# Optimization experiments

Hardware: AMD Instinct MI355X
Metric: run time of the kernel (lower is better)

Reference implementation:

```python
import jax, jax.numpy as jnp
import numpy as np

N = 50000        # nodes
E = 800000       # edges
FEAT = 64        # cfg.feature_dim
HID = 128        # cfg.hidden_dim
G = 8            # num graphs
EPS = 1e-5       # LayerNorm eps
MIN_DEPTH, MAX_DEPTH = 0.1, 3.0


def _ln(x, g, b):
    m = jnp.mean(x, axis=-1, keepdims=True)
    v = jnp.mean((x - m) ** 2, axis=-1, keepdims=True)
    return (x - m) * jax.lax.rsqrt(v + EPS) * g + b


def setup_inputs() -> dict:
    key = jax.random.key(0)
    ks = jax.random.split(key, 32)
    f32 = jnp.float32
    inp = {}
    inp['x'] = jax.random.normal(ks[0], (N, FEAT), dtype=f32)
    inp['edge_index'] = jax.random.randint(ks[1], (2, E), 0, N)
    inp['batch'] = jnp.sort(jax.random.randint(ks[2], (N,), 0, G))
    # input_projection: Linear(FEAT,HID) + LayerNorm
    inp['in_w'] = jax.random.normal(ks[3], (FEAT, HID), dtype=f32) * (1.0 / np.sqrt(FEAT))
    inp['in_b'] = jnp.zeros((HID,), f32)
    inp['in_ln_g'] = jnp.ones((HID,), f32)
    inp['in_ln_b'] = jnp.zeros((HID,), f32)
    # epigenetics
    inp['methylation'] = jnp.zeros((HID,), f32)
    inp['histones'] = jnp.zeros((4,), f32)
    inp['log_depth'] = jnp.zeros((), f32)
    # NeuralODEFunc: 3 stacked GCNConv(HID,HID) + LayerNorms, gate MLP, residual scalar
    inp['gcn_w'] = jax.random.normal(ks[4], (3, HID, HID), dtype=f32) * (1.0 / np.sqrt(HID))
    inp['gcn_b'] = jnp.zeros((3, HID), f32)
    inp['ln_g'] = jnp.ones((3, HID), f32)
    inp['ln_b'] = jnp.zeros((3, HID), f32)
    inp['gate_w'] = jax.random.normal(ks[5], (2 * HID, HID), dtype=f32) * (1.0 / np.sqrt(2 * HID))
    inp['gate_b'] = jnp.zeros((HID,), f32)
    inp['residual_weight'] = jnp.asarray(0.1, f32)
    # output_projection: Linear(HID,HID) + LayerNorm
    inp['out_w'] = jax.random.normal(ks[6], (HID, HID), dtype=f32) * (1.0 / np.sqrt(HID))
    inp['out_b'] = jnp.zeros((HID,), f32)
    inp['out_ln_g'] = jnp.ones((HID,), f32)
    inp['out_ln_b'] = jnp.zeros((HID,), f32)
    return inp


def reference(x, edge_index, batch, in_w, in_b, in_ln_g, in_ln_b, methylation,
              histones, log_depth, gcn_w, gcn_b, ln_g, ln_b, gate_w, gate_b,
              residual_weight, out_w, out_b, out_ln_g, out_ln_b):
    n = x.shape[0]
    src, dst = edge_index[0], edge_index[1]

    # input_projection (Dropout is identity in eval)
    h = jax.nn.relu(_ln(x @ in_w + in_b, in_ln_g, in_ln_b))

    # epigenetic regulation (chromatin_accessibility goes through .item() -> constant)
    meth_sil = jnp.mean(jax.nn.sigmoid(methylation))
    hm = jax.nn.sigmoid(histones)
    act = (hm[0] + hm[2]) * 0.5
    rep = (hm[1] + hm[3]) * 0.5
    chrom = jax.lax.stop_gradient(jnp.clip(act - rep + 0.5, 0.0, 1.0))
    h = h * (chrom * (1.0 - meth_sil))

    # symmetric GCN normalization, no self loops (computed once, no grad path)
    deg = jax.ops.segment_sum(jnp.ones((E,), h.dtype), dst, num_segments=n)
    dinv = jnp.where(deg > 0, jax.lax.rsqrt(jnp.maximum(deg, 1.0)), 0.0)
    enorm = (dinv[src] * dinv[dst])[:, None]  # [E,1]

    def gcn(hh, i):
        xw = hh @ gcn_w[i]                                   # [N,H]
        agg = jax.ops.segment_sum(xw[src] * enorm, dst, num_segments=n)
        return agg + gcn_b[i]

    def ode_f(hh):
        h_orig = hh
        cur = hh
        for i in range(3):  # fixed layer count
            h_new = _ln(gcn(cur, i), ln_g[i], ln_b[i])
            if i > 0:
                gate = jax.nn.sigmoid(
                    jnp.concatenate([cur, h_new], axis=-1) @ gate_w + gate_b)
                cur = gate * h_new + (1.0 - gate) * cur
            else:
                cur = h_new
        cur = jnp.tanh(cur)
        return cur + residual_weight * h_orig

    # depth via .item() in torch -> non-differentiable constant
    depth = jax.lax.stop_gradient(
        jnp.clip(jnp.exp(log_depth), MIN_DEPTH, MAX_DEPTH))
    # single fixed RK4 step over t = linspace(0, depth, 2)
    dt = depth
    k1 = ode_f(h)
    k2 = ode_f(h + 0.5 * dt * k1)
    k3 = ode_f(h + 0.5 * dt * k2)
    k4 = ode_f(h + dt * k3)
    h_final = h + (dt / 6.0) * (k1 + 2.0 * k2 + 2.0 * k3 + k4)

    # output_projection + global_mean_pool over batch
    h_out = _ln(h_final @ out_w + out_b, out_ln_g, out_ln_b)
    cnt = jax.ops.segment_sum(jnp.ones((n,), h.dtype), batch, num_segments=G)
    pooled = jax.ops.segment_sum(h_out, batch, num_segments=G)
    return pooled / jnp.maximum(cnt, 1.0)[:, None]
```

## Files before the change

kernel.cpp:

```cpp
#include <hip/hip_runtime.h>
#include <math.h>

#define NN 50000
#define EE 800000
#define HH 128
#define FF 64
#define GG 8
#define PB 500
#define SB 1600

using short8 = __attribute__((ext_vector_type(8))) short;
using f32x4  = __attribute__((ext_vector_type(4))) float;
using f32x2  = __attribute__((ext_vector_type(2))) float;

__device__ __forceinline__ float sigm(float x){ return 1.0f/(1.0f+expf(-x)); }
__device__ __forceinline__ unsigned short f2bf(float f){
    union { float f; unsigned u; } v; v.f = f;
    unsigned r = v.u + 0x7fff + ((v.u >> 16) & 1);
    return (unsigned short)(r >> 16);
}
__device__ __forceinline__ float bf2f(unsigned short h){
    union { unsigned u; float f; } v; v.u = ((unsigned)h) << 16;
    return v.f;
}

#if __has_builtin(__builtin_amdgcn_cvt_pk_fp8_f32) && __has_builtin(__builtin_amdgcn_cvt_pk_f32_fp8)
#define FP8_HW 1
#else
#define FP8_HW 0
#endif

__device__ __forceinline__ unsigned fp8enc1_sw(float f){
    union { float fl; unsigned u; } x; x.fl = f;
    unsigned s = (x.u >> 31) << 7;
    float a = fabsf(f);
    if (!(a > 0.f)) return s;
    if (a >= 448.f) return s | 0x7E;
    if (a < 0.015625f) {
        int q = (int)(a * 512.f + 0.5f);
        if (q > 7) return s | (1u << 3);
        return s | (unsigned)q;
    }
    unsigned u = x.u + (1u << 19);
    int e32 = (int)((u >> 23) & 255) - 127;
    if (e32 < -6) { int q=(int)(a*512.f+0.5f); if(q>7)q=7; return s|(unsigned)q; }
    if (e32 > 8) return s | 0x7E;
    unsigned m = (u >> 20) & 7;
    return s | ((unsigned)(e32 + 7) << 3) | m;
}
__device__ __forceinline__ float fp8dec1_sw(unsigned v){
    unsigned s = v >> 7, e = (v >> 3) & 15, m = v & 7;
    float f;
    if (e == 0) f = (float)m * 0.001953125f;
    else { union { unsigned u; float fl; } x; x.u = ((e + 120u) << 23) | (m << 20); f = x.fl; }
    return s ? -f : f;
}
__device__ __forceinline__ unsigned char e2fp8(float a){
#if FP8_HW
    return (unsigned char)(__builtin_amdgcn_cvt_pk_fp8_f32(a, a, 0, false) & 0xFF);
#else
    return (unsigned char)fp8enc1_sw(a);
#endif
}
__device__ __forceinline__ unsigned pk4fp8(float a, float b, float c, float d){
#if FP8_HW
    unsigned p0 = (unsigned)__builtin_amdgcn_cvt_pk_fp8_f32(a, b, 0, false);
    unsigned p1 = (unsigned)__builtin_amdgcn_cvt_pk_fp8_f32(c, d, 0, false);
    return (p0 & 0xFFFFu) | ((p1 & 0xFFFFu) << 16);
#else
    return fp8enc1_sw(a) | (fp8enc1_sw(b) << 8) | (fp8enc1_sw(c) << 16) | (fp8enc1_sw(d) << 24);
#endif
}
__device__ __forceinline__ float2 d2fp8(unsigned short u){
#if FP8_HW
    f32x2 r = __builtin_amdgcn_cvt_pk_f32_fp8((int)(unsigned)u, false);
    return make_float2(r[0], r[1]);
#else
    return make_float2(fp8dec1_sw(u & 0xFF), fp8dec1_sw((u >> 8) & 0xFF));
#endif
}

__global__ void k_setup(const float* __restrict__ meth,
                        const float* __restrict__ histones,
                        const float* __restrict__ logd,
                        float* __restrict__ scal,
                        const int* __restrict__ batch, int* __restrict__ st)
{
    if (blockIdx.x == 1) {
        int g = threadIdx.x;
        if (g > GG) return;
        int lo = 0, hi = NN;
        while (lo < hi) { int mid = (lo + hi) >> 1; if (batch[mid] < g) lo = mid + 1; else hi = mid; }
        st[g] = lo;
        return;
    }
    int l = threadIdx.x;
    float s = sigm(meth[l]) + sigm(meth[l + 64]);
#pragma unroll
    for (int o = 32; o >= 1; o >>= 1) s += __shfl_xor(s, o, 64);
    if (l == 0) {
        float msil = s * (1.0f / 128.0f);
        float h0 = sigm(histones[0]), h1 = sigm(histones[1]);
        float h2 = sigm(histones[2]), h3 = sigm(histones[3]);
        float act = (h0 + h2) * 0.5f, rep = (h1 + h3) * 0.5f;
        float chrom = fminf(fmaxf(act - rep + 0.5f, 0.0f), 1.0f);
        scal[0] = chrom * (1.0f - msil);
        float d = expf(logd[0]);
        scal[1] = fminf(fmaxf(d, 0.1f), 3.0f);
    }
}

__global__ void k_packall(const float* __restrict__ in_w, const float* __restrict__ gcn_w,
                          const float* __restrict__ gate_w, const float* __restrict__ out_w,
                          unsigned short* __restrict__ outp)
{
    int i = blockIdx.x * 256 + threadIdx.x;
    if (i >= 8192 + 6 * 16384) return;
    const float* src; int base, li;
    if (i < 8192) { src = in_w + i; base = 0; li = i; }
    else {
        int j = i - 8192;
        int m = j >> 14, r = j & 16383;
        base = 8192 + (m << 14); li = r;
        if (m < 3)      src = gcn_w  + m * 16384 + r;
        else if (m < 5) src = gate_w + (m - 3) * 16384 + r;
        else            src = out_w + r;
    }
    int k = li >> 7, n = li & 127;
    int c = k >> 5, kl = k & 31, q = kl >> 3, j2 = kl & 7;
    int b = n >> 4, ln = n & 15;
    int lane = q * 16 + ln;
    outp[base + ((c * 8 + b) * 64 + lane) * 8 + j2] = f2bf(*src);
}

__global__ void k_cvtx(const float* __restrict__ x, unsigned short* __restrict__ xb)
{
    size_t i = (size_t)blockIdx.x * 256 + threadIdx.x;
    if (i >= (size_t)NN * 16) return;
    float4 v = ((const float4*)x)[i];
    ushort4 o;
    o.x = f2bf(v.x); o.y = f2bf(v.y); o.z = f2bf(v.z); o.w = f2bf(v.w);
    ((ushort4*)xb)[i] = o;
}

__global__ void k_hist(const int* __restrict__ ei, int* __restrict__ hist)
{
    int e = blockIdx.x * 256 + threadIdx.x;
    if (e < EE) atomicAdd(&hist[ei[EE + e]], 1);
}

__global__ void k_dinv(const int* __restrict__ hist, float* __restrict__ dinv)
{
    int n = blockIdx.x * 256 + threadIdx.x;
    if (n < NN) {
        int d = hist[n];
        dinv[n] = d > 0 ? rsqrtf((float)d) : 0.0f;
    }
}

__global__ void k_scan_a(const int* __restrict__ hist, int* __restrict__ aux)
{
    __shared__ int sh[256];
    int b = blockIdx.x, t = threadIdx.x;
    int base = b * 1024 + t * 4;
    int s = 0;
#pragma unroll
    for (int j = 0; j < 4; ++j) { int i = base + j; if (i < NN) s += hist[i]; }
    sh[t] = s; __syncthreads();
    for (int o = 128; o >= 1; o >>= 1) { if (t < o) sh[t] += sh[t + o]; __syncthreads(); }
    if (t == 0) aux[b] = sh[0];
}

__global__ void k_scan_b(int* __restrict__ aux, int nb)
{
    if (blockIdx.x == 0 && threadIdx.x == 0) {
        int run = 0;
        for (int i = 0; i < nb; ++i) { int v = aux[i]; aux[i] = run; run += v; }
    }
}

__global__ void k_scan_c(const int* __restrict__ hist, const int* __restrict__ aux,
                         int* __restrict__ row_ptr)
{
    __shared__ int sh[256];
    int b = blockIdx.x, t = threadIdx.x;
    int base = b * 1024 + t * 4;
    int v[4]; int s = 0;
#pragma unroll
    for (int j = 0; j < 4; ++j) { int i = base + j; v[j] = (i < NN) ? hist[i] : 0; s += v[j]; }
    sh[t] = s; __syncthreads();
    for (int o = 1; o < 256; o <<= 1) {
        int x = 0; if (t >= o) x = sh[t - o];
        __syncthreads(); sh[t] += x; __syncthreads();
    }
    int run = aux[b] + sh[t] - s;
#pragma unroll
    for (int j = 0; j < 4; ++j) { int i = base + j; if (i < NN) row_ptr[i] = run; run += v[j]; }
    if (b == 0 && t == 0) row_ptr[NN] = EE;
}

__global__ __launch_bounds__(256) void k_scatter(const int* __restrict__ ei,
                          const float* __restrict__ dinv,
                          int* __restrict__ cursor, uint2* __restrict__ ew)
{
    if (blockIdx.x == 0 && threadIdx.x < 128)
        ew[EE + threadIdx.x] = make_uint2(0u, 0u);
    const int grp = blockIdx.x & 7;
    const int blk = blockIdx.x >> 3;
    const int CH  = EE / (SB / 8);
    const int e0 = blk * CH, e1 = e0 + CH;
    const int glo = grp * (NN / 8), ghi = glo + (NN / 8);
    for (int e = e0 + threadIdx.x; e < e1; e += 256) {
        int d = ei[EE + e];
        if (d >= glo && d < ghi) {
            int s = ei[e];
            int p = atomicAdd(&cursor[d], 1);
            ew[p] = make_uint2((unsigned)(s & 0xFFFF) | ((unsigned)(d & 15) << 16),
                               __float_as_uint(dinv[s] * dinv[d]));
        }
    }
}

template<int KC, int MODE>
__global__ __launch_bounds__(256) void k_dense_mfma(
    const unsigned short* __restrict__ A, const unsigned short* __restrict__ Wp,
    const float* __restrict__ bias, const float* __restrict__ lng,
    const float* __restrict__ lnb, const float* __restrict__ scal,
    unsigned short* __restrict__ out, unsigned char* __restrict__ out8)
{
    __shared__ unsigned short Ws[KC * 4096];
    const int t = threadIdx.x;
    {
        const float4* src = (const float4*)Wp;
        float4* dst = (float4*)Ws;
#pragma unroll
        for (int i = 0; i < KC * 2; ++i) dst[t + i * 256] = src[t + i * 256];
    }
    __syncthreads();
    const int wave = t >> 6, lane = t & 63;
    const int quad = lane >> 4, ln = lane & 15;
    const int r0 = blockIdx.x * 64 + wave * 16;
    const int K = KC * 32;
    const int arow = r0 + ln;
    const bool av = arow < NN;

    f32x4 acc[8] = {};
#pragma unroll
    for (int c = 0; c < KC; ++c) {
        short8 a = {};
        if (av) a = *(const short8*)(A + (size_t)arow * K + c * 32 + quad * 8);
#pragma unroll
        for (int b = 0; b < 8; ++b) {
            short8 bb = *(const short8*)&Ws[((c * 8 + b) * 64 + lane) * 8];
            acc[b] = __builtin_amdgcn_mfma_f32_16x16x32_bf16(a, bb, acc[b], 0, 0, 0);
        }
    }

    float b_s[8], g_s[8], e_s[8];
#pragma unroll
    for (int b = 0; b < 8; ++b) {
        int col = b * 16 + ln;
        b_s[b] = bias[col]; g_s[b] = lng[col]; e_s[b] = lnb[col];
    }
    float sc = (MODE == 1) ? scal[0] : 0.0f;
#pragma unroll
    for (int i = 0; i < 4; ++i) {
        int row = r0 + quad * 4 + i;
        float v[8]; float s = 0.f, q = 0.f;
#pragma unroll
        for (int b = 0; b < 8; ++b) { float x = acc[b][i] + b_s[b]; v[b] = x; s += x; q += x * x; }
#pragma unroll
        for (int o = 1; o < 16; o <<= 1) { s += __shfl_xor(s, o, 64); q += __shfl_xor(q, o, 64); }
        float m  = s * (1.0f / 128.0f);
        float vr = q * (1.0f / 128.0f) - m * m;
        float rs = rsqrtf(vr + 1e-5f);
        if (row < NN) {
#pragma unroll
            for (int b = 0; b < 8; ++b) {
                float o2 = (v[b] - m) * rs * g_s[b] + e_s[b];
                if (MODE == 1) o2 = fmaxf(o2, 0.f) * sc;
                out[(size_t)row * 128 + b * 16 + ln] = f2bf(o2);
                if (out8) out8[(size_t)row * 128 + b * 16 + ln] = e2fp8(o2);
            }
        }
    }
}

__global__ __launch_bounds__(128) void k_spgemm(
    const int* __restrict__ rp, const uint2* __restrict__ ew,
    const unsigned char* __restrict__ X8, const unsigned short* __restrict__ Wp,
    const float* __restrict__ bias, const float* __restrict__ lng,
    const float* __restrict__ lnb, unsigned short* __restrict__ out,
    unsigned char* __restrict__ out8)
{
    __shared__ float accf[2][16 * 132];
    const int t = threadIdx.x, wave = t >> 6, lane = t & 63;
    const int quad = lane >> 4, ln = lane & 15;
    const int half = lane >> 5, li = lane & 31;
    const int n0 = blockIdx.x * 16;
    const int nf = n0 + wave * 8;

    {
        float* z0 = &accf[0][wave * 8 * 132];
        float* z1 = &accf[1][wave * 8 * 132];
        for (int i = lane; i < 8 * 132; i += 64) { z0[i] = 0.f; z1[i] = 0.f; }
    }

    if (nf < NN) {
        const int nl = min(nf + 8, NN);
        const int ebeg = __builtin_amdgcn_readfirstlane(rp[nf]);
        const int eend = __builtin_amdgcn_readfirstlane(rp[nl]);
        if (ebeg < eend) {
            float4 racc = make_float4(0.f, 0.f, 0.f, 0.f);
            int curd = (int)((ew[min(ebeg + half, eend - 1)].x >> 16) & 15u);
            const unsigned char* Xl = X8 + li * 4;
            uint2 rec[8], recN[8]; unsigned g[8];
#pragma unroll
            for (int j = 0; j < 8; ++j) rec[j]  = ew[ebeg + 2 * j + half];
#pragma unroll
            for (int j = 0; j < 8; ++j) recN[j] = ew[ebeg + 16 + 2 * j + half];
#pragma unroll
            for (int j = 0; j < 8; ++j) {
                int src = (int)(rec[j].x & 0xFFFFu);
                g[j] = *(const unsigned*)(Xl + (size_t)src * 128);
            }
            for (int e = ebeg; e < eend; e += 16) {
                unsigned gN[8]; uint2 recNN[8];
#pragma unroll
                for (int j = 0; j < 8; ++j) {
                    int src = (int)(recN[j].x & 0xFFFFu);
                    gN[j] = *(const unsigned*)(Xl + (size_t)src * 128);
                }
#pragma unroll
                for (int j = 0; j < 8; ++j) recNN[j] = ew[e + 32 + 2 * j + half];
                int lim = eend - e;
                int mj = lim > half ? ((lim - half + 1) >> 1) : 0; if (mj > 8) mj = 8;
#pragma unroll
                for (int j = 0; j < 8; ++j) {
                    if (j >= mj) break;
                    float wgt = __uint_as_float(rec[j].y);
                    int dl = (int)((rec[j].x >> 16) & 15u);
                    if (dl != curd) {
                        *(float4*)&accf[half][curd * 132 + li * 4] = racc;
                        racc = make_float4(0.f, 0.f, 0.f, 0.f);
                        curd = dl;
                    }
                    float2 p0 = d2fp8((unsigned short)(g[j] & 0xFFFFu));
                    float2 p1 = d2fp8((unsigned short)(g[j] >> 16));
                    racc.x = fmaf(wgt, p0.x, racc.x);
                    racc.y = fmaf(wgt, p0.y, racc.y);
                    racc.z = fmaf(wgt, p1.x, racc.z);
                    racc.w = fmaf(wgt, p1.y, racc.w);
                }
#pragma unroll
                for (int j = 0; j < 8; ++j) { rec[j] = recN[j]; recN[j] = recNN[j]; g[j] = gN[j]; }
            }
            *(float4*)&accf[half][curd * 132 + li * 4] = racc;
        }
    }
    __syncthreads();

    f32x4 acc[8] = {};
    const float* ar0 = &accf[0][(size_t)ln * 132];
    const float* ar1 = &accf[1][(size_t)ln * 132];
#pragma unroll
    for (int c = 0; c < 4; ++c) {
        float4 a0 = *(const float4*)(ar0 + c * 32 + quad * 8);
        float4 a1 = *(const float4*)(ar0 + c * 32 + quad * 8 + 4);
        float4 b0 = *(const float4*)(ar1 + c * 32 + quad * 8);
        float4 b1 = *(const float4*)(ar1 + c * 32 + quad * 8 + 4);
        short8 af;
        af[0] = (short)f2bf(a0.x + b0.x); af[1] = (short)f2bf(a0.y + b0.y);
        af[2] = (short)f2bf(a0.z + b0.z); af[3] = (short)f2bf(a0.w + b0.w);
        af[4] = (short)f2bf(a1.x + b1.x); af[5] = (short)f2bf(a1.y + b1.y);
        af[6] = (short)f2bf(a1.z + b1.z); af[7] = (short)f2bf(a1.w + b1.w);
#pragma unroll
        for (int b = 0; b < 8; ++b) {
            short8 bb = *(const short8*)(Wp + ((size_t)(c * 8 + b) * 64 + lane) * 8);
            acc[b] = __builtin_amdgcn_mfma_f32_16x16x32_bf16(af, bb, acc[b], 0, 0, 0);
        }
    }

    float b_s[8], g_s[8], e_s[8];
#pragma unroll
    for (int b = 0; b < 8; ++b) {
        int col = b * 16 + ln;
        b_s[b] = bias[col]; g_s[b] = lng[col]; e_s[b] = lnb[col];
    }
#pragma unroll
    for (int i = 0; i < 4; ++i) {
        int row = n0 + quad * 4 + i;
        float v[8]; float s = 0.f, q = 0.f;
#pragma unroll
        for (int b = 0; b < 8; ++b) { float x = acc[b][i] + b_s[b]; v[b] = x; s += x; q += x * x; }
#pragma unroll
        for (int o = 1; o < 16; o <<= 1) { s += __shfl_xor(s, o, 64); q += __shfl_xor(q, o, 64); }
        float m  = s * (1.0f / 128.0f);
        float vr = q * (1.0f / 128.0f) - m * m;
        float rs = rsqrtf(vr + 1e-5f);
        if (((quad >> 1) == wave) && row < NN) {
#pragma unroll
            for (int b = 0; b < 8; ++b) {
                float o2 = (v[b] - m) * rs * g_s[b] + e_s[b];
                out[(size_t)row * 128 + b * 16 + ln] = f2bf(o2);
                if (out8) out8[(size_t)row * 128 + b * 16 + ln] = e2fp8(o2);
            }
        }
    }
}

__global__ __launch_bounds__(256) void k_gate_mfma(
    unsigned short* __restrict__ cur, const unsigned short* __restrict__ hnew,
    const unsigned short* __restrict__ Wp, const float* __restrict__ gb,
    unsigned char* __restrict__ cur8)
{
    __shared__ unsigned short Ws[16384];
    const int t = threadIdx.x;
    const int wave = t >> 6, lane = t & 63;
    const int quad = lane >> 4, ln = lane & 15;
    const int r0 = blockIdx.x * 64 + wave * 16;
    const int arow = r0 + ln;
    const bool av = arow < NN;

    f32x4 acc[8] = {};
#pragma unroll
    for (int s = 0; s < 2; ++s) {
        __syncthreads();
        {
            const float4* src = (const float4*)(Wp + (size_t)s * 16384);
            float4* dst = (float4*)Ws;
#pragma unroll
            for (int i = 0; i < 8; ++i) dst[t + i * 256] = src[t + i * 256];
        }
        __syncthreads();
        const unsigned short* A = s ? hnew : cur;
#pragma unroll
        for (int c = 0; c < 4; ++c) {
            short8 a = {};
            if (av) a = *(const short8*)(A + (size_t)arow * 128 + c * 32 + quad * 8);
#pragma unroll
            for (int b = 0; b < 8; ++b) {
                short8 bb = *(const short8*)&Ws[((c * 8 + b) * 64 + lane) * 8];
                acc[b] = __builtin_amdgcn_mfma_f32_16x16x32_bf16(a, bb, acc[b], 0, 0, 0);
            }
        }
    }

    float gb_s[8];
#pragma unroll
    for (int b = 0; b < 8; ++b) gb_s[b] = gb[b * 16 + ln];
#pragma unroll
    for (int i = 0; i < 4; ++i) {
        int row = r0 + quad * 4 + i;
        if (row < NN) {
#pragma unroll
            for (int b = 0; b < 8; ++b) {
                size_t idx = (size_t)row * 128 + b * 16 + ln;
                float g  = sigm(acc[b][i] + gb_s[b]);
                float cu = bf2f(cur[idx]);
                float hn = bf2f(hnew[idx]);
                float r  = g * hn + (1.f - g) * cu;
                cur[idx]  = f2bf(r);
                cur8[idx] = e2fp8(r);
            }
        }
    }
}

template<int S>
__global__ __launch_bounds__(256) void k_gate_fused(
    const unsigned short* __restrict__ cur, const unsigned short* __restrict__ hnew,
    const unsigned short* __restrict__ Wp, const float* __restrict__ gb,
    const unsigned short* __restrict__ fin, const unsigned short* __restrict__ h0,
    float* __restrict__ acc, unsigned short* __restrict__ ybuf,
    unsigned char* __restrict__ y8, const float* __restrict__ scal,
    const float* __restrict__ rwp)
{
    __shared__ unsigned short Ws[16384];
    const int t = threadIdx.x;
    const int wave = t >> 6, lane = t & 63;
    const int quad = lane >> 4, ln = lane & 15;
    const int r0 = blockIdx.x * 64 + wave * 16;
    const int arow = r0 + ln;
    const bool av = arow < NN;

    f32x4 am[8] = {};
#pragma unroll
    for (int s = 0; s < 2; ++s) {
        __syncthreads();
        {
            const float4* src = (const float4*)(Wp + (size_t)s * 16384);
            float4* dst = (float4*)Ws;
#pragma unroll
            for (int i = 0; i < 8; ++i) dst[t + i * 256] = src[t + i * 256];
        }
        __syncthreads();
        const unsigned short* A = s ? hnew : cur;
#pragma unroll
        for (int c = 0; c < 4; ++c) {
            short8 a = {};
            if (av) a = *(const short8*)(A + (size_t)arow * 128 + c * 32 + quad * 8);
#pragma unroll
            for (int b = 0; b < 8; ++b) {
                short8 bb = *(const short8*)&Ws[((c * 8 + b) * 64 + lane) * 8];
                am[b] = __builtin_amdgcn_mfma_f32_16x16x32_bf16(a, bb, am[b], 0, 0, 0);
            }
        }
    }

    float gb_s[8];
#pragma unroll
    for (int b = 0; b < 8; ++b) gb_s[b] = gb[b * 16 + ln];
    const float dt = scal[1], rw = rwp[0];
    const float wk = (S == 1 || S == 4) ? dt * (1.f / 6.f) : dt * (1.f / 3.f);
    const float cn = (S == 3) ? dt : 0.5f * dt;
#pragma unroll
    for (int i = 0; i < 4; ++i) {
        int row = r0 + quad * 4 + i;
        if (row < NN) {
#pragma unroll
            for (int b = 0; b < 8; ++b) {
                size_t idx = (size_t)row * 128 + b * 16 + ln;
                float g  = sigm(am[b][i] + gb_s[b]);
                float cu = bf2f(cur[idx]);
                float hn = bf2f(hnew[idx]);
                float r  = g * hn + (1.f - g) * cu;
                float tv = tanhf(r) + rw * bf2f(fin[idx]);
                float a  = (S == 1) ? wk * tv : acc[idx] + wk * tv;
                acc[idx] = a;
                float yv = (S == 4) ? bf2f(h0[idx]) + a
                                    : bf2f(h0[idx]) + cn * tv;
                ybuf[idx] = f2bf(yv);
                y8[idx]   = e2fp8(yv);
            }
        }
    }
}

__global__ __launch_bounds__(128) void k_pool1(
    const unsigned short* __restrict__ h, const int* __restrict__ batch,
    float* __restrict__ partial)
{
    int c = threadIdx.x, b = blockIdx.x;
    int r0 = b * (NN / PB), r1 = r0 + (NN / PB);
    float acc = 0.f;
    int gfirst = batch[r0], g = gfirst;
#pragma unroll 4
    for (int r = r0; r < r1; ++r) {
        int gg = batch[r];
        if (gg != g) {
            partial[(size_t)b * 1024 + g * 128 + c] = acc;
            for (int z = g + 1; z < gg; ++z) partial[(size_t)b * 1024 + z * 128 + c] = 0.f;
            acc = 0.f; g = gg;
        }
        acc += bf2f(h[(size_t)r * 128 + c]);
    }
    partial[(size_t)b * 1024 + g * 128 + c] = acc;
    for (int z = 0; z < gfirst; ++z)  partial[(size_t)b * 1024 + z * 128 + c] = 0.f;
    for (int z = g + 1; z < GG; ++z)  partial[(size_t)b * 1024 + z * 128 + c] = 0.f;
}

__global__ __launch_bounds__(256) void k_pool2(
    const float* __restrict__ partial, const int* __restrict__ st,
    float* __restrict__ out)
{
    __shared__ float sh[8][32];
    int cb = blockIdx.x & 3, g = blockIdx.x >> 2;
    int cl = threadIdx.x & 31, sl = threadIdx.x >> 5;
    int c = cb * 32 + cl;
    float s = 0.f;
    for (int b = sl; b < PB; b += 8) s += partial[(size_t)b * 1024 + g * 128 + c];
    sh[sl][cl] = s; __syncthreads();
    if (sl == 0) {
        float tt = 0.f;
#pragma unroll
        for (int i = 0; i < 8; ++i) tt += sh[i][cl];
        int cnt = st[g + 1] - st[g];
        out[g * 128 + c] = tt / (float)(cnt > 0 ? cnt : 1);
    }
}

static inline size_t al(size_t x) { return (x + 255) & ~(size_t)255; }

extern "C" void kernel_launch(void* const* d_in, const int* in_sizes, int n_in,
                              void* d_out, int out_size, void* d_ws, size_t ws_size,
                              hipStream_t stream)
{
    const float* x       = (const float*)d_in[0];
    const int*   ei      = (const int*)d_in[1];
    const int*   batch   = (const int*)d_in[2];
    const float* in_w    = (const float*)d_in[3];
    const float* in_b    = (const float*)d_in[4];
    const float* in_lng  = (const float*)d_in[5];
    const float* in_lnb  = (const float*)d_in[6];
    const float* meth    = (const float*)d_in[7];
    const float* histn   = (const float*)d_in[8];
    const float* logd    = (const float*)d_in[9];
    const float* gcn_w   = (const float*)d_in[10];
    const float* gcn_b   = (const float*)d_in[11];
    const float* ln_g    = (const float*)d_in[12];
    const float* ln_b    = (const float*)d_in[13];
    const float* gate_w  = (const float*)d_in[14];
    const float* gate_b  = (const float*)d_in[15];
    const float* rw      = (const float*)d_in[16];
    const float* out_w   = (const float*)d_in[17];
    const float* out_b   = (const float*)d_in[18];
    const float* out_lng = (const float*)d_in[19];
    const float* out_lnb = (const float*)d_in[20];
    float* out = (float*)d_out;

    char* w = (char*)d_ws;
    size_t off = 0;
    float* scal   = (float*)(w + off); off += al(16 * 4);
    int*   hist   = (int*)(w + off);   off += al((size_t)NN * 4);
    int*   rp     = (int*)(w + off);   off += al((size_t)(NN + 1) * 4);
    int*   cursor = (int*)(w + off);   off += al((size_t)(NN + 1) * 4);
    int*   aux    = (int*)(w + off);   off += al(64 * 4);
    int*   st     = (int*)(w + off);   off += al(16 * 4);
    float* dinv   = (float*)(w + off); off += al((size_t)NN * 4);
    uint2* ew     = (uint2*)(w + off); off += al((size_t)(EE + 128) * 8);
    float* partial= (float*)(w + off); off += al((size_t)PB * 1024 * 4);
    unsigned short* wpak = (unsigned short*)(w + off); off += al((size_t)(8192 + 6 * 16384) * 2);
    unsigned short* inwp  = wpak;
    unsigned short* gcnwp = wpak + 8192;
    unsigned short* gwp   = wpak + 8192 + 3 * 16384;
    unsigned short* owp   = wpak + 8192 + 5 * 16384;
    size_t B16 = al((size_t)NN * 128 * 2);
    unsigned short* xb  = (unsigned short*)(w + off); off += al((size_t)NN * 64 * 2);
    unsigned short* h0  = (unsigned short*)(w + off); off += B16;
    unsigned short* y   = (unsigned short*)(w + off); off += B16;
    unsigned short* cur = (unsigned short*)(w + off); off += B16;
    unsigned short* t2  = (unsigned short*)(w + off); off += B16;
    float* acc = (float*)(w + off); off += al((size_t)NN * 128 * 4);
    size_t B8 = al((size_t)NN * 128);
    unsigned char* h08  = (unsigned char*)(w + off); off += B8;
    unsigned char* y8   = (unsigned char*)(w + off); off += B8;
    unsigned char* cur8 = (unsigned char*)(w + off); off += B8;
    if (off > ws_size) return;

    hipMemsetAsync(hist, 0, (size_t)NN * 4, stream);

    k_setup<<<2, 64, 0, stream>>>(meth, histn, logd, scal, batch, st);
    k_packall<<<(8192 + 6 * 16384 + 255) / 256, 256, 0, stream>>>(in_w, gcn_w, gate_w, out_w, wpak);
    k_cvtx<<<3125, 256, 0, stream>>>(x, xb);

    k_hist<<<(EE + 255) / 256, 256, 0, stream>>>(ei, hist);
    k_dinv<<<(NN + 255) / 256, 256, 0, stream>>>(hist, dinv);
    k_scan_a<<<49, 256, 0, stream>>>(hist, aux);
    k_scan_b<<<1, 1, 0, stream>>>(aux, 49);
    k_scan_c<<<49, 256, 0, stream>>>(hist, aux, rp);
    hipMemcpyAsync(cursor, rp, (size_t)(NN + 1) * 4, hipMemcpyDeviceToDevice, stream);
    k_scatter<<<SB, 256, 0, stream>>>(ei, dinv, cursor, ew);

    const int DG = (NN + 63) / 64;
    const int SG = (NN + 15) / 16;
    k_dense_mfma<2, 1><<<DG, 256, 0, stream>>>(xb, inwp, in_b, in_lng, in_lnb, scal, h0, h08);

    for (int s = 1; s <= 4; ++s) {
        const unsigned short* fin = (s == 1) ? h0 : y;
        const unsigned char*  fin8 = (s == 1) ? h08 : y8;
        k_spgemm<<<SG, 128, 0, stream>>>(rp, ew, fin8, gcnwp, gcn_b, ln_g, ln_b, cur, cur8);
        k_spgemm<<<SG, 128, 0, stream>>>(rp, ew, cur8,
                                         gcnwp + (size_t)1 * 128 * 128, gcn_b + 128,
                                         ln_g + 128, ln_b + 128, t2, (unsigned char*)0);
        k_gate_mfma<<<DG, 256, 0, stream>>>(cur, t2, gwp, gate_b, cur8);
        k_spgemm<<<SG, 128, 0, stream>>>(rp, ew, cur8,
                                         gcnwp + (size_t)2 * 128 * 128, gcn_b + 256,
                                         ln_g + 256, ln_b + 256, t2, (unsigned char*)0);
        if (s == 1)      k_gate_fused<1><<<DG, 256, 0, stream>>>(cur, t2, gwp, gate_b, fin, h0, acc, y, y8, scal, rw);
        else if (s == 2) k_gate_fused<2><<<DG, 256, 0, stream>>>(cur, t2, gwp, gate_b, fin, h0, acc, y, y8, scal, rw);
        else if (s == 3) k_gate_fused<3><<<DG, 256, 0, stream>>>(cur, t2, gwp, gate_b, fin, h0, acc, y, y8, scal, rw);
        else             k_gate_fused<4><<<DG, 256, 0, stream>>>(cur, t2, gwp, gate_b, fin, h0, acc, y, y8, scal, rw);
    }

    k_dense_mfma<4, 0><<<DG, 256, 0, stream>>>(y, owp, out_b, out_lng, out_lnb, scal, t2, (unsigned char*)0);
    k_pool1<<<PB, 128, 0, stream>>>(t2, batch, partial);
    k_pool2<<<GG * 4, 256, 0, stream>>>(partial, st, out);
}
```

Before: 881.0 us.

## Factor GCN edge norm into per-node scaling and shrink edge records

```diff
diff --git a/kernel.cpp b/kernel.cpp
--- a/kernel.cpp
+++ b/kernel.cpp
@@ -7,7 +7,6 @@
 #define FF 64
 #define GG 8
 #define PB 500
-#define SB 1600
 
 using short8 = __attribute__((ext_vector_type(8))) short;
 using f32x4  = __attribute__((ext_vector_type(4))) float;
@@ -60,15 +59,6 @@
     return (unsigned char)(__builtin_amdgcn_cvt_pk_fp8_f32(a, a, 0, false) & 0xFF);
 #else
     return (unsigned char)fp8enc1_sw(a);
-#endif
-}
-__device__ __forceinline__ unsigned pk4fp8(float a, float b, float c, float d){
-#if FP8_HW
-    unsigned p0 = (unsigned)__builtin_amdgcn_cvt_pk_fp8_f32(a, b, 0, false);
-    unsigned p1 = (unsigned)__builtin_amdgcn_cvt_pk_fp8_f32(c, d, 0, false);
-    return (p0 & 0xFFFFu) | ((p1 & 0xFFFFu) << 16);
-#else
-    return fp8enc1_sw(a) | (fp8enc1_sw(b) << 8) | (fp8enc1_sw(c) << 16) | (fp8enc1_sw(d) << 24);
 #endif
 }
 __device__ __forceinline__ float2 d2fp8(unsigned short u){
@@ -200,24 +190,16 @@
 }
 
 __global__ __launch_bounds__(256) void k_scatter(const int* __restrict__ ei,
-                          const float* __restrict__ dinv,
-                          int* __restrict__ cursor, uint2* __restrict__ ew)
+                          int* __restrict__ cursor, unsigned* __restrict__ ew)
 {
     if (blockIdx.x == 0 && threadIdx.x < 128)
-        ew[EE + threadIdx.x] = make_uint2(0u, 0u);
-    const int grp = blockIdx.x & 7;
-    const int blk = blockIdx.x >> 3;
-    const int CH  = EE / (SB / 8);
-    const int e0 = blk * CH, e1 = e0 + CH;
-    const int glo = grp * (NN / 8), ghi = glo + (NN / 8);
-    for (int e = e0 + threadIdx.x; e < e1; e += 256) {
+        ew[EE + threadIdx.x] = 0u;
+    int e = blockIdx.x * 256 + threadIdx.x;
+    if (e < EE) {
         int d = ei[EE + e];
-        if (d >= glo && d < ghi) {
-            int s = ei[e];
-            int p = atomicAdd(&cursor[d], 1);
-            ew[p] = make_uint2((unsigned)(s & 0xFFFF) | ((unsigned)(d & 15) << 16),
-                               __float_as_uint(dinv[s] * dinv[d]));
-        }
+        int s = ei[e];
+        int p = atomicAdd(&cursor[d], 1);
+        ew[p] = (unsigned)s | ((unsigned)(d & 15) << 16);
     }
 }
 
@@ -226,6 +208,7 @@
     const unsigned short* __restrict__ A, const unsigned short* __restrict__ Wp,
     const float* __restrict__ bias, const float* __restrict__ lng,
     const float* __restrict__ lnb, const float* __restrict__ scal,
+    const float* __restrict__ dinv,
     unsigned short* __restrict__ out, unsigned char* __restrict__ out8)
 {
     __shared__ unsigned short Ws[KC * 4096];
@@ -275,23 +258,24 @@
         float vr = q * (1.0f / 128.0f) - m * m;
         float rs = rsqrtf(vr + 1e-5f);
         if (row < NN) {
+            float dv = out8 ? dinv[row] : 0.f;
 #pragma unroll
             for (int b = 0; b < 8; ++b) {
                 float o2 = (v[b] - m) * rs * g_s[b] + e_s[b];
                 if (MODE == 1) o2 = fmaxf(o2, 0.f) * sc;
                 out[(size_t)row * 128 + b * 16 + ln] = f2bf(o2);
-                if (out8) out8[(size_t)row * 128 + b * 16 + ln] = e2fp8(o2);
+                if (out8) out8[(size_t)row * 128 + b * 16 + ln] = e2fp8(o2 * dv);
             }
         }
     }
 }
 
 __global__ __launch_bounds__(128) void k_spgemm(
-    const int* __restrict__ rp, const uint2* __restrict__ ew,
+    const int* __restrict__ rp, const unsigned* __restrict__ ew,
     const unsigned char* __restrict__ X8, const unsigned short* __restrict__ Wp,
     const float* __restrict__ bias, const float* __restrict__ lng,
-    const float* __restrict__ lnb, unsigned short* __restrict__ out,
-    unsigned char* __restrict__ out8)
+    const float* __restrict__ lnb, const float* __restrict__ dinv,
+    unsigned short* __restrict__ out, unsigned char* __restrict__ out8)
 {
     __shared__ float accf[2][16 * 132];
     const int t = threadIdx.x, wave = t >> 6, lane = t & 63;
@@ -312,23 +296,23 @@
         const int eend = __builtin_amdgcn_readfirstlane(rp[nl]);
         if (ebeg < eend) {
             float4 racc = make_float4(0.f, 0.f, 0.f, 0.f);
-            int curd = (int)((ew[min(ebeg + half, eend - 1)].x >> 16) & 15u);
+            int curd = (int)((ew[min(ebeg + half, eend - 1)] >> 16) & 15u);
             const unsigned char* Xl = X8 + li * 4;
-            uint2 rec[8], recN[8]; unsigned g[8];
+            unsigned rec[8], recN[8], g[8];
 #pragma unroll
             for (int j = 0; j < 8; ++j) rec[j]  = ew[ebeg + 2 * j + half];
 #pragma unroll
             for (int j = 0; j < 8; ++j) recN[j] = ew[ebeg + 16 + 2 * j + half];
 #pragma unroll
             for (int j = 0; j < 8; ++j) {
-                int src = (int)(rec[j].x & 0xFFFFu);
+                int src = (int)(rec[j] & 0xFFFFu);
                 g[j] = *(const unsigned*)(Xl + (size_t)src * 128);
             }
             for (int e = ebeg; e < eend; e += 16) {
-                unsigned gN[8]; uint2 recNN[8];
+                unsigned gN[8], recNN[8];
 #pragma unroll
                 for (int j = 0; j < 8; ++j) {
-                    int src = (int)(recN[j].x & 0xFFFFu);
+                    int src = (int)(recN[j] & 0xFFFFu);
                     gN[j] = *(const unsigned*)(Xl + (size_t)src * 128);
                 }
 #pragma unroll
@@ -338,8 +322,7 @@
 #pragma unroll
                 for (int j = 0; j < 8; ++j) {
                     if (j >= mj) break;
-                    float wgt = __uint_as_float(rec[j].y);
-                    int dl = (int)((rec[j].x >> 16) & 15u);
+                    int dl = (int)((rec[j] >> 16) & 15u);
                     if (dl != curd) {
                         *(float4*)&accf[half][curd * 132 + li * 4] = racc;
                         racc = make_float4(0.f, 0.f, 0.f, 0.f);
@@ -347,10 +330,10 @@
                     }
                     float2 p0 = d2fp8((unsigned short)(g[j] & 0xFFFFu));
                     float2 p1 = d2fp8((unsigned short)(g[j] >> 16));
-                    racc.x = fmaf(wgt, p0.x, racc.x);
-                    racc.y = fmaf(wgt, p0.y, racc.y);
-                    racc.z = fmaf(wgt, p1.x, racc.z);
-                    racc.w = fmaf(wgt, p1.y, racc.w);
+                    racc.x += p0.x;
+                    racc.y += p0.y;
+                    racc.z += p1.x;
+                    racc.w += p1.y;
                 }
 #pragma unroll
                 for (int j = 0; j < 8; ++j) { rec[j] = recN[j]; recN[j] = recNN[j]; g[j] = gN[j]; }
@@ -390,9 +373,10 @@
 #pragma unroll
     for (int i = 0; i < 4; ++i) {
         int row = n0 + quad * 4 + i;
+        float dv = (row < NN) ? dinv[row] : 0.f;
         float v[8]; float s = 0.f, q = 0.f;
 #pragma unroll
-        for (int b = 0; b < 8; ++b) { float x = acc[b][i] + b_s[b]; v[b] = x; s += x; q += x * x; }
+        for (int b = 0; b < 8; ++b) { float x = acc[b][i] * dv + b_s[b]; v[b] = x; s += x; q += x * x; }
 #pragma unroll
         for (int o = 1; o < 16; o <<= 1) { s += __shfl_xor(s, o, 64); q += __shfl_xor(q, o, 64); }
         float m  = s * (1.0f / 128.0f);
@@ -403,7 +387,7 @@
             for (int b = 0; b < 8; ++b) {
                 float o2 = (v[b] - m) * rs * g_s[b] + e_s[b];
                 out[(size_t)row * 128 + b * 16 + ln] = f2bf(o2);
-                if (out8) out8[(size_t)row * 128 + b * 16 + ln] = e2fp8(o2);
+                if (out8) out8[(size_t)row * 128 + b * 16 + ln] = e2fp8(o2 * dv);
             }
         }
     }
@@ -412,7 +396,7 @@
 __global__ __launch_bounds__(256) void k_gate_mfma(
     unsigned short* __restrict__ cur, const unsigned short* __restrict__ hnew,
     const unsigned short* __restrict__ Wp, const float* __restrict__ gb,
-    unsigned char* __restrict__ cur8)
+    const float* __restrict__ dinv, unsigned char* __restrict__ cur8)
 {
     __shared__ unsigned short Ws[16384];
     const int t = threadIdx.x;
@@ -453,6 +437,7 @@
     for (int i = 0; i < 4; ++i) {
         int row = r0 + quad * 4 + i;
         if (row < NN) {
+            float dv = dinv[row];
 #pragma unroll
             for (int b = 0; b < 8; ++b) {
                 size_t idx = (size_t)row * 128 + b * 16 + ln;
@@ -461,7 +446,7 @@
                 float hn = bf2f(hnew[idx]);
                 float r  = g * hn + (1.f - g) * cu;
                 cur[idx]  = f2bf(r);
-                cur8[idx] = e2fp8(r);
+                cur8[idx] = e2fp8(r * dv);
             }
         }
     }
@@ -474,7 +459,7 @@
     const unsigned short* __restrict__ fin, const unsigned short* __restrict__ h0,
     float* __restrict__ acc, unsigned short* __restrict__ ybuf,
     unsigned char* __restrict__ y8, const float* __restrict__ scal,
-    const float* __restrict__ rwp)
+    const float* __restrict__ rwp, const float* __restrict__ dinv)
 {
     __shared__ unsigned short Ws[16384];
     const int t = threadIdx.x;
@@ -518,6 +503,7 @@
     for (int i = 0; i < 4; ++i) {
         int row = r0 + quad * 4 + i;
         if (row < NN) {
+            float dv = dinv[row];
 #pragma unroll
             for (int b = 0; b < 8; ++b) {
                 size_t idx = (size_t)row * 128 + b * 16 + ln;
@@ -531,7 +517,7 @@
                 float yv = (S == 4) ? bf2f(h0[idx]) + a
                                     : bf2f(h0[idx]) + cn * tv;
                 ybuf[idx] = f2bf(yv);
-                y8[idx]   = e2fp8(yv);
+                y8[idx]   = e2fp8(yv * dv);
             }
         }
     }
@@ -618,7 +604,7 @@
     int*   aux    = (int*)(w + off);   off += al(64 * 4);
     int*   st     = (int*)(w + off);   off += al(16 * 4);
     float* dinv   = (float*)(w + off); off += al((size_t)NN * 4);
-    uint2* ew     = (uint2*)(w + off); off += al((size_t)(EE + 128) * 8);
+    unsigned* ew  = (unsigned*)(w + off); off += al((size_t)(EE + 128) * 4);
     float* partial= (float*)(w + off); off += al((size_t)PB * 1024 * 4);
     unsigned short* wpak = (unsigned short*)(w + off); off += al((size_t)(8192 + 6 * 16384) * 2);
     unsigned short* inwp  = wpak;
@@ -650,30 +636,30 @@
     k_scan_b<<<1, 1, 0, stream>>>(aux, 49);
     k_scan_c<<<49, 256, 0, stream>>>(hist, aux, rp);
     hipMemcpyAsync(cursor, rp, (size_t)(NN + 1) * 4, hipMemcpyDeviceToDevice, stream);
-    k_scatter<<<SB, 256, 0, stream>>>(ei, dinv, cursor, ew);
+    k_scatter<<<(EE + 255) / 256, 256, 0, stream>>>(ei, cursor, ew);
 
     const int DG = (NN + 63) / 64;
     const int SG = (NN + 15) / 16;
-    k_dense_mfma<2, 1><<<DG, 256, 0, stream>>>(xb, inwp, in_b, in_lng, in_lnb, scal, h0, h08);
+    k_dense_mfma<2, 1><<<DG, 256, 0, stream>>>(xb, inwp, in_b, in_lng, in_lnb, scal, dinv, h0, h08);
 
     for (int s = 1; s <= 4; ++s) {
         const unsigned short* fin = (s == 1) ? h0 : y;
         const unsigned char*  fin8 = (s == 1) ? h08 : y8;
-        k_spgemm<<<SG, 128, 0, stream>>>(rp, ew, fin8, gcnwp, gcn_b, ln_g, ln_b, cur, cur8);
+        k_spgemm<<<SG, 128, 0, stream>>>(rp, ew, fin8, gcnwp, gcn_b, ln_g, ln_b, dinv, cur, cur8);
         k_spgemm<<<SG, 128, 0, stream>>>(rp, ew, cur8,
                                          gcnwp + (size_t)1 * 128 * 128, gcn_b + 128,
-                                         ln_g + 128, ln_b + 128, t2, (unsigned char*)0);
-        k_gate_mfma<<<DG, 256, 0, stream>>>(cur, t2, gwp, gate_b, cur8);
+                                         ln_g + 128, ln_b + 128, dinv, t2, (unsigned char*)0);
+        k_gate_mfma<<<DG, 256, 0, stream>>>(cur, t2, gwp, gate_b, dinv, cur8);
         k_spgemm<<<SG, 128, 0, stream>>>(rp, ew, cur8,
                                          gcnwp + (size_t)2 * 128 * 128, gcn_b + 256,
-                                         ln_g + 256, ln_b + 256, t2, (unsigned char*)0);
-        if (s == 1)      k_gate_fused<1><<<DG, 256, 0, stream>>>(cur, t2, gwp, gate_b, fin, h0, acc, y, y8, scal, rw);
-        else if (s == 2) k_gate_fused<2><<<DG, 256, 0, stream>>>(cur, t2, gwp, gate_b, fin, h0, acc, y, y8, scal, rw);
-        else if (s == 3) k_gate_fused<3><<<DG, 256, 0, stream>>>(cur, t2, gwp, gate_b, fin, h0, acc, y, y8, scal, rw);
-        else             k_gate_fused<4><<<DG, 256, 0, stream>>>(cur, t2, gwp, gate_b, fin, h0, acc, y, y8, scal, rw);
-    }
-
-    k_dense_mfma<4, 0><<<DG, 256, 0, stream>>>(y, owp, out_b, out_lng, out_lnb, scal, t2, (unsigned char*)0);
+                                         ln_g + 256, ln_b + 256, dinv, t2, (unsigned char*)0);
+        if (s == 1)      k_gate_fused<1><<<DG, 256, 0, stream>>>(cur, t2, gwp, gate_b, fin, h0, acc, y, y8, scal, rw, dinv);
+        else if (s == 2) k_gate_fused<2><<<DG, 256, 0, stream>>>(cur, t2, gwp, gate_b, fin, h0, acc, y, y8, scal, rw, dinv);
+        else if (s == 3) k_gate_fused<3><<<DG, 256, 0, stream>>>(cur, t2, gwp, gate_b, fin, h0, acc, y, y8, scal, rw, dinv);
+        else             k_gate_fused<4><<<DG, 256, 0, stream>>>(cur, t2, gwp, gate_b, fin, h0, acc, y, y8, scal, rw, dinv);
+    }
+
+    k_dense_mfma<4, 0><<<DG, 256, 0, stream>>>(y, owp, out_b, out_lng, out_lnb, scal, dinv, t2, (unsigned char*)0);
     k_pool1<<<PB, 128, 0, stream>>>(t2, batch, partial);
     k_pool2<<<GG * 4, 256, 0, stream>>>(partial, st, out);
 }
```

New measurement: 857.1 us. -2.7%, faster.
